# Kernel tuning notes

Hardware: AMD Instinct MI355X
Metric: run time of the kernel (lower is better)

The kernel has to match this reference:

```python
import jax, jax.numpy as jnp
import numpy as np

B = 32768
PASSES = 4

# mask layout: (batch, digit, row, col), values in {0,1}

def _to_lines(m, d):
    """Reorder so the last axis enumerates the 9 cells of a line and axis -2 the 9 lines."""
    if d == 'h':
        return m                      # lines = rows, cells = cols
    if d == 'v':
        return jnp.swapaxes(m, 2, 3)  # lines = cols, cells = rows
    b = m.shape[0]                    # lines = 3x3 boxes
    return m.reshape(b, 9, 3, 3, 3, 3).transpose(0, 1, 2, 4, 3, 5).reshape(b, 9, 9, 9)

_from_lines = _to_lines  # all three reorderings are self-inverse


def filter_line(m, d):
    """SudokuFilterHVBox: remove a solved cell's digit from all other cells in its line."""
    l = _to_lines(m, d)
    cnt = l.sum(axis=1, keepdims=True)                 # candidates per cell
    solved = l * (cnt == 1).astype(l.dtype)            # one-hot solved cells
    other = solved.sum(axis=-1, keepdims=True) - solved  # same digit solved elsewhere in line
    out = l * (other == 0).astype(l.dtype)
    return _from_lines(out, d)


def unique_line(m, d):
    """SudokuUniqueHVBox (hidden single): if a digit fits only one cell in a line, fix it."""
    l = _to_lines(m, d)
    cnt_line = l.sum(axis=-1, keepdims=True)           # per-digit count in the line
    hidden = l * (cnt_line == 1).astype(l.dtype)       # lone placements
    has = hidden.sum(axis=1, keepdims=True) > 0        # cell hosts a hidden single
    out = jnp.where(has, hidden, l)
    return _from_lines(out, d)


def doubles_line(m, d):
    """SudokuDigitsDoubles (naked pair): two identical 2-candidate cells in a line
    eliminate those digits from the rest of the line."""
    l = _to_lines(m, d)                                # (B, d, line, cell)
    cnt = l.sum(axis=1, keepdims=True)
    pm = l * (cnt == 2).astype(l.dtype)                # patterns of 2-candidate cells
    dot = jnp.einsum('bdlc,bdle->blce', pm, pm)        # pattern overlap between cells
    eye = jnp.eye(9, dtype=l.dtype)
    match = (dot == 2).astype(l.dtype) * (1.0 - eye)   # identical pair at another cell
    pairflag = match.sum(-1) > 0                       # (B, line, cell) part of a naked pair
    pair_digit = pm * pairflag[:, None, :, :].astype(l.dtype)
    total_pd = pair_digit.sum(-1, keepdims=True)       # digit belongs to some pair in line
    remove = (total_pd > 0) & (pair_digit == 0)
    out = l * (1.0 - remove.astype(l.dtype))
    return _from_lines(out, d)


def pointing(m, d):
    """SudokuDigitsInOneLineAtBox: if a digit's box candidates lie in one row/col,
    remove that digit from the rest of the row/col outside the box."""
    b = m.shape[0]
    v = m.reshape(b, 9, 3, 3, 3, 3)                    # (B, d, br, ri, bc, ci)
    if d == 'h':
        pres = v.sum(axis=5) > 0                       # (B,d,br,ri,bc) digit in row of box
        nrows = pres.sum(axis=3, keepdims=True)
        point = pres & (nrows == 1)                    # confined to single row within box
        tot = point.sum(axis=4, keepdims=True)         # over bc
        rem = (tot - point) > 0                        # pointing from another box hits us
        out = v * (1.0 - rem[..., None].astype(v.dtype))
    else:
        pres = v.sum(axis=3) > 0                       # (B,d,br,bc,ci) digit in col of box
        ncols = pres.sum(axis=4, keepdims=True)
        point = pres & (ncols == 1)
        tot = point.sum(axis=2, keepdims=True)         # over br
        rem = (tot - point) > 0
        out = v * (1.0 - rem[:, :, :, None, :, :].astype(v.dtype))
    return out.reshape(b, 9, 9, 9)


def _forward_mask(mask):
    for _ in range(PASSES):
        mask = filter_line(mask, 'box')
        mask = pointing(mask, 'h')
        mask = pointing(mask, 'v')
        mask = unique_line(mask, 'h')
        mask = unique_line(mask, 'v')
        mask = unique_line(mask, 'box')
        mask = doubles_line(mask, 'v')   # original code instantiates doubles_h with 'v'
        mask = doubles_line(mask, 'v')
        mask = doubles_line(mask, 'box')
    return mask


def setup_inputs() -> dict:
    key = jax.random.key(0)
    mask = jax.random.randint(key, (B, 9, 9, 9), 0, 2).astype(jnp.float32)
    return {"mask": mask}


def reference(mask):
    out = _forward_mask(mask)
    cnt = out.sum(axis=1)                              # candidates per cell
    solved = jnp.all(cnt == 1, axis=(1, 2))            # (B,) puzzle fully determined
    return (out, solved)
```

## Files before the change

### kernel.cpp

```cpp
#include <hip/hip_runtime.h>
#include <stdint.h>

#define NB 32768
#define NPASS 4
#define FULL27 0x07FFFFFFu
#define NBF (NB * 729)


__device__ __forceinline__ uint32_t colfold(uint32_t w) {
    return (w | (w >> 9) | (w >> 18)) & 0x1FFu;
}
__device__ __forceinline__ uint32_t colmaj2(uint32_t w) {
    return ((w & (w >> 9)) | ((w | (w >> 9)) & (w >> 18))) & 0x1FFu;
}

__global__ __launch_bounds__(256, 1)
void sudoku_kernel(const uint32_t* __restrict__ in, float* __restrict__ out,
                   float* __restrict__ solved) {
    __shared__ uint32_t bpool[1920];
    const int lane = threadIdx.x & 63;
    const int wv   = threadIdx.x >> 6;
    const int trip = lane / 3;
    const int band = lane - trip * 3;
    const int bo1 = band == 2 ? 0 : band + 1;
    const int bo2 = band == 0 ? 2 : band - 1;
    int sl1 = trip * 3 + bo1; if (sl1 > 63) sl1 = 63;
    int sl2 = trip * 3 + bo2; if (sl2 > 63) sl2 = 63;
    const int blockP = blockIdx.x * 84;
    const int pb = blockP + wv * 21;
    const int p = pb + trip;
    const bool valid = (trip < 21) && (p < NB);

    {
        const int base = pb * 729;
        uint32_t* mypool = &bpool[wv * 480];
        #pragma unroll 1
        for (int c = 0; c < 15; ++c) {
            uint32_t v[16];
            #pragma unroll
            for (int j = 0; j < 16; ++j) {
                int gi = base + (c * 16 + j) * 64 + lane;
                if (gi >= NBF) gi = NBF - 1;
                v[j] = in[gi];
            }
            #pragma unroll
            for (int j = 0; j < 16; ++j) {
                unsigned long long m = __ballot(v[j] != 0u);
                if (lane == 0) {
                    int r = c * 16 + j;
                    mypool[2 * r]     = (uint32_t)m;
                    mypool[2 * r + 1] = (uint32_t)(m >> 32);
                }
            }
        }
    }
    __syncthreads();

    uint32_t bd[9];
    {
        const uint32_t* mypool = &bpool[wv * 480];
        const int tx = trip > 20 ? 20 : trip;
        const int bb0 = tx * 729 + band * 27;
        #pragma unroll
        for (int d = 0; d < 9; ++d) {
            int bb = bb0 + d * 81;
            int di = bb >> 5, sh = bb & 31;
            uint64_t both = (uint64_t)mypool[di] | ((uint64_t)mypool[di + 1] << 32);
            bd[d] = (uint32_t)(both >> sh) & FULL27;
        }
    }
    __syncthreads();

    #pragma unroll 1
    for (int pass = 0; pass < NPASS; ++pass) {
        {
            uint32_t on = 0, tw = 0, fo = 0;
            #pragma unroll
            for (int d = 0; d < 9; ++d) {
                uint32_t c = on & bd[d];
                on ^= bd[d]; fo |= tw & c; tw ^= c;
            }
            uint32_t ex1 = on & ~tw & ~fo;
            #pragma unroll
            for (int d = 0; d < 9; ++d) {
                uint32_t s = bd[d] & ex1;
                #pragma unroll
                for (int k = 0; k < 3; ++k) {
                    uint32_t bm = 0x1C0E07u << (3 * k);
                    uint32_t sm = s & bm;
                    uint32_t multi = sm & (sm - 1u);
                    uint32_t keep = (sm == 0u) ? 0xFFFFFFFFu : (~bm | (multi ? 0u : sm));
                    bd[d] &= keep;
                }
            }
        }

        #pragma unroll
        for (int d = 0; d < 9; ++d) {
            uint32_t w = bd[d];
            uint32_t t = (w | (w >> 1) | (w >> 2)) & 0x01249249u;
            uint32_t sum = (t & 0x1FFu) + ((t >> 9) & 0x1FFu) + ((t >> 18) & 0x1FFu);
            uint32_t single = sum & ~(sum >> 1) & 0x49u;
            uint32_t point = t & (single * 0x40201u);
            uint32_t clearm = 0;
            #pragma unroll
            for (int r = 0; r < 3; ++r) {
                uint32_t pr = (point >> (9 * r)) & 0x1FFu;
                uint32_t multi = pr & (pr - 1u);
                uint32_t segkeep = multi ? 0u : pr * 7u;
                uint32_t rc = pr ? ((0x1FFu & ~segkeep) << (9 * r)) : 0u;
                clearm |= rc;
            }
            bd[d] = w & ~clearm;
        }

        {
            uint32_t pnt[9];
            #pragma unroll
            for (int d = 0; d < 9; ++d) {
                uint32_t w = bd[d];
                uint32_t q = colfold(w);
                uint32_t u = (q & 0x49u) + ((q >> 1) & 0x49u) + ((q >> 2) & 0x49u);
                uint32_t single = u & ~(u >> 1) & 0x49u;
                pnt[d] = q & (single * 7u);
            }
            #pragma unroll
            for (int d = 0; d < 9; ++d) {
                uint32_t o = (uint32_t)__shfl((int)pnt[d], sl1, 64) |
                             (uint32_t)__shfl((int)pnt[d], sl2, 64);
                bd[d] &= ~(o * 0x40201u);
            }
        }

        {
            uint32_t hid[9], has = 0;
            #pragma unroll
            for (int d = 0; d < 9; ++d) {
                uint32_t w = bd[d], h = 0;
                #pragma unroll
                for (int r = 0; r < 3; ++r) {
                    uint32_t x = w & (0x1FFu << (9 * r));
                    h |= (x & (x - 1u)) ? 0u : x;
                }
                hid[d] = h; has |= h;
            }
            #pragma unroll
            for (int d = 0; d < 9; ++d) bd[d] = (bd[d] & ~has) | hid[d];
        }

        {
            uint32_t hid[9], has = 0;
            #pragma unroll
            for (int d = 0; d < 9; ++d) {
                uint32_t w = bd[d];
                uint32_t q0 = colfold(w), m0 = colmaj2(w);
                uint32_t ex = q0 | (m0 << 9);
                uint32_t ea = (uint32_t)__shfl((int)ex, sl1, 64);
                uint32_t eb = (uint32_t)__shfl((int)ex, sl2, 64);
                uint32_t qa = ea & 0x1FFu, ma = ea >> 9;
                uint32_t qb = eb & 0x1FFu, mb = eb >> 9;
                uint32_t ge2 = m0 | ma | mb | (q0 & qa) | (q0 & qb) | (qa & qb);
                uint32_t ex1c = (q0 | qa | qb) & ~ge2;
                hid[d] = w & ((ex1c & q0) * 0x40201u);
                has |= hid[d];
            }
            #pragma unroll
            for (int d = 0; d < 9; ++d) bd[d] = (bd[d] & ~has) | hid[d];
        }

        {
            uint32_t hid[9], has = 0;
            #pragma unroll
            for (int d = 0; d < 9; ++d) {
                uint32_t w = bd[d], h = 0;
                #pragma unroll
                for (int k = 0; k < 3; ++k) {
                    uint32_t x = w & (0x1C0E07u << (3 * k));
                    h |= (x & (x - 1u)) ? 0u : x;
                }
                hid[d] = h; has |= h;
            }
            #pragma unroll
            for (int d = 0; d < 9; ++d) bd[d] = (bd[d] & ~has) | hid[d];
        }

        #pragma unroll 1
        for (int rep = 0; rep < 2; ++rep) {
            uint32_t on = 0, tw = 0, fo = 0;
            #pragma unroll
            for (int d = 0; d < 9; ++d) {
                uint32_t c = on & bd[d];
                on ^= bd[d]; fo |= tw & c; tw ^= c;
            }
            uint32_t ex2 = tw & ~on & ~fo;
            uint32_t Q[9], K[9];
            #pragma unroll
            for (int d = 0; d < 9; ++d) { Q[d] = bd[d] & ex2; K[d] = 0u; }
            #pragma unroll
            for (int d1 = 0; d1 < 9; ++d1)
                #pragma unroll
                for (int d2 = d1 + 1; d2 < 9; ++d2) {
                    uint32_t P = Q[d1] & Q[d2];
                    uint32_t f0 = colfold(P), g0 = colmaj2(P);
                    uint32_t ex = f0 | (g0 << 9);
                    uint32_t ea = (uint32_t)__shfl((int)ex, sl1, 64);
                    uint32_t eb = (uint32_t)__shfl((int)ex, sl2, 64);
                    uint32_t fa = ea & 0x1FFu, ga = ea >> 9;
                    uint32_t fb = eb & 0x1FFu, gb = eb >> 9;
                    uint32_t dup = g0 | ga | gb | (f0 & fa) | (f0 & fb) | (fa & fb);
                    uint32_t sK = P & (dup * 0x40201u);
                    K[d1] |= sK; K[d2] |= sK;
                }
            #pragma unroll
            for (int d = 0; d < 9; ++d) {
                uint32_t kc = colfold(K[d]);
                uint32_t cols = kc | (uint32_t)__shfl((int)kc, sl1, 64)
                                   | (uint32_t)__shfl((int)kc, sl2, 64);
                uint32_t em = cols * 0x40201u;
                bd[d] = (bd[d] & ~em) | K[d];
            }
        }

        {
            uint32_t on = 0, tw = 0, fo = 0;
            #pragma unroll
            for (int d = 0; d < 9; ++d) {
                uint32_t c = on & bd[d];
                on ^= bd[d]; fo |= tw & c; tw ^= c;
            }
            uint32_t ex2 = tw & ~on & ~fo;
            uint32_t Q[9], K[9];
            #pragma unroll
            for (int d = 0; d < 9; ++d) { Q[d] = bd[d] & ex2; K[d] = 0u; }
            #pragma unroll
            for (int d1 = 0; d1 < 9; ++d1)
                #pragma unroll
                for (int d2 = d1 + 1; d2 < 9; ++d2) {
                    uint32_t P = Q[d1] & Q[d2];
                    #pragma unroll
                    for (int k = 0; k < 3; ++k) {
                        uint32_t m = P & (0x1C0E07u << (3 * k));
                        uint32_t s = (m & (m - 1u)) ? m : 0u;
                        K[d1] |= s; K[d2] |= s;
                    }
                }
            #pragma unroll
            for (int d = 0; d < 9; ++d)
                #pragma unroll
                for (int k = 0; k < 3; ++k) {
                    uint32_t bm = 0x1C0E07u << (3 * k);
                    uint32_t t = K[d] & bm;
                    uint32_t mask = t ? (~bm | t) : 0xFFFFFFFFu;
                    bd[d] &= mask;
                }
        }
    }

    {
        uint32_t on = 0, tw = 0, fo = 0;
        #pragma unroll
        for (int d = 0; d < 9; ++d) {
            uint32_t c = on & bd[d];
            on ^= bd[d]; fo |= tw & c; tw ^= c;
        }
        uint32_t okb = ((on & ~tw & ~fo) == FULL27) ? 1u : 0u;
        uint32_t all = okb & (uint32_t)__shfl((int)okb, sl1, 64)
                           & (uint32_t)__shfl((int)okb, sl2, 64);
        if (valid && band == 0) solved[p] = all ? 1.0f : 0.0f;
    }

    for (int j = threadIdx.x; j < 1914; j += 256) bpool[j] = 0u;
    __syncthreads();
    if (valid) {
        const int pbit = (wv * 21 + trip) * 729;
        #pragma unroll
        for (int d = 0; d < 9; ++d) {
            int bitbase = pbit + d * 81 + band * 27;
            int di = bitbase >> 5;
            int sh = bitbase & 31;
            uint64_t both = (uint64_t)bd[d] << sh;
            atomicOr(&bpool[di], (uint32_t)both);
            atomicOr(&bpool[di + 1], (uint32_t)(both >> 32));
        }
    }
    __syncthreads();
    {
        int nvb = NB - blockP; if (nvb > 84) nvb = 84;
        const int limit4 = nvb * 729 / 4;
        float4* dst4 = (float4*)(out + (size_t)blockP * 729);
        #pragma unroll 4
        for (int i = 0; i < 60; ++i) {
            int j = i * 256 + (int)threadIdx.x;
            if (j < limit4) {
                uint32_t nib = (bpool[j >> 3] >> ((j & 7) * 4)) & 0xFu;
                dst4[j] = make_float4((float)(nib & 1u), (float)((nib >> 1) & 1u),
                                      (float)((nib >> 2) & 1u), (float)((nib >> 3) & 1u));
            }
        }
    }
}

extern "C" void kernel_launch(void* const* d_in, const int* in_sizes, int n_in,
                              void* d_out, int out_size, void* d_ws, size_t ws_size,
                              hipStream_t stream) {
    const uint32_t* in = (const uint32_t*)d_in[0];
    float* out = (float*)d_out;
    float* solved = out + (size_t)NB * 729;
    sudoku_kernel<<<(NB + 83) / 84, 256, 0, stream>>>(in, out, solved);
}
```

Baseline: 217.0 us.

## Use single-wave blocks with 20 puzzles each instead of 4-wave blocks

Restructures the launch from 256-thread blocks handling 84 puzzles (21 per wave) to 64-thread single-wave blocks handling 20 puzzles each. The load loop is adjusted to cover exactly 20 puzzles' bits (14 chunks plus a 4-row tail), and the output store uses one wave. This raises the block count and lets waves run independently without block-wide syncs across four waves, improving scheduling and latency hiding, at the cost of fewer lanes used per wave (60 of 64 instead of 63).

```diff
diff --git a/kernel.cpp b/kernel.cpp
--- a/kernel.cpp
+++ b/kernel.cpp
@@ -5,6 +5,8 @@
 #define NPASS 4
 #define FULL27 0x07FFFFFFu
 #define NBF (NB * 729)
+#define PPW 20
+#define NBLK ((NB + PPW - 1) / PPW)
 
 
 __device__ __forceinline__ uint32_t colfold(uint32_t w) {
@@ -14,28 +16,25 @@
     return ((w & (w >> 9)) | ((w | (w >> 9)) & (w >> 18))) & 0x1FFu;
 }
 
-__global__ __launch_bounds__(256, 1)
+__global__ __launch_bounds__(64)
 void sudoku_kernel(const uint32_t* __restrict__ in, float* __restrict__ out,
                    float* __restrict__ solved) {
-    __shared__ uint32_t bpool[1920];
-    const int lane = threadIdx.x & 63;
-    const int wv   = threadIdx.x >> 6;
+    __shared__ uint32_t pool[460];
+    const int lane = threadIdx.x;
     const int trip = lane / 3;
     const int band = lane - trip * 3;
     const int bo1 = band == 2 ? 0 : band + 1;
     const int bo2 = band == 0 ? 2 : band - 1;
     int sl1 = trip * 3 + bo1; if (sl1 > 63) sl1 = 63;
     int sl2 = trip * 3 + bo2; if (sl2 > 63) sl2 = 63;
-    const int blockP = blockIdx.x * 84;
-    const int pb = blockP + wv * 21;
-    const int p = pb + trip;
-    const bool valid = (trip < 21) && (p < NB);
+    const int p0 = blockIdx.x * PPW;
+    const int p = p0 + trip;
+    const bool valid = (trip < PPW) && (p < NB);
 
     {
-        const int base = pb * 729;
-        uint32_t* mypool = &bpool[wv * 480];
+        const int base = p0 * 729;
         #pragma unroll 1
-        for (int c = 0; c < 15; ++c) {
+        for (int c = 0; c < 14; ++c) {
             uint32_t v[16];
             #pragma unroll
             for (int j = 0; j < 16; ++j) {
@@ -48,8 +47,26 @@
                 unsigned long long m = __ballot(v[j] != 0u);
                 if (lane == 0) {
                     int r = c * 16 + j;
-                    mypool[2 * r]     = (uint32_t)m;
-                    mypool[2 * r + 1] = (uint32_t)(m >> 32);
+                    pool[2 * r]     = (uint32_t)m;
+                    pool[2 * r + 1] = (uint32_t)(m >> 32);
+                }
+            }
+        }
+        {
+            uint32_t v[4];
+            #pragma unroll
+            for (int j = 0; j < 4; ++j) {
+                int gi = base + (224 + j) * 64 + lane;
+                if (gi >= NBF) gi = NBF - 1;
+                v[j] = in[gi];
+            }
+            #pragma unroll
+            for (int j = 0; j < 4; ++j) {
+                unsigned long long m = __ballot(v[j] != 0u);
+                if (lane == 0) {
+                    int r = 224 + j;
+                    pool[2 * r]     = (uint32_t)m;
+                    pool[2 * r + 1] = (uint32_t)(m >> 32);
                 }
             }
         }
@@ -58,14 +75,13 @@
 
     uint32_t bd[9];
     {
-        const uint32_t* mypool = &bpool[wv * 480];
-        const int tx = trip > 20 ? 20 : trip;
+        const int tx = trip >= PPW ? PPW - 1 : trip;
         const int bb0 = tx * 729 + band * 27;
         #pragma unroll
         for (int d = 0; d < 9; ++d) {
             int bb = bb0 + d * 81;
             int di = bb >> 5, sh = bb & 31;
-            uint64_t both = (uint64_t)mypool[di] | ((uint64_t)mypool[di + 1] << 32);
+            uint64_t both = (uint64_t)pool[di] | ((uint64_t)pool[di + 1] << 32);
             bd[d] = (uint32_t)(both >> sh) & FULL27;
         }
     }
@@ -269,30 +285,30 @@
         if (valid && band == 0) solved[p] = all ? 1.0f : 0.0f;
     }
 
-    for (int j = threadIdx.x; j < 1914; j += 256) bpool[j] = 0u;
+    for (int j = lane; j < 456; j += 64) pool[j] = 0u;
     __syncthreads();
     if (valid) {
-        const int pbit = (wv * 21 + trip) * 729;
+        const int pbit = trip * 729;
         #pragma unroll
         for (int d = 0; d < 9; ++d) {
             int bitbase = pbit + d * 81 + band * 27;
             int di = bitbase >> 5;
             int sh = bitbase & 31;
             uint64_t both = (uint64_t)bd[d] << sh;
-            atomicOr(&bpool[di], (uint32_t)both);
-            atomicOr(&bpool[di + 1], (uint32_t)(both >> 32));
+            atomicOr(&pool[di], (uint32_t)both);
+            atomicOr(&pool[di + 1], (uint32_t)(both >> 32));
         }
     }
     __syncthreads();
     {
-        int nvb = NB - blockP; if (nvb > 84) nvb = 84;
-        const int limit4 = nvb * 729 / 4;
-        float4* dst4 = (float4*)(out + (size_t)blockP * 729);
+        int nv = NB - p0; if (nv > PPW) nv = PPW;
+        const int limit4 = nv * 729 / 4;
+        float4* dst4 = (float4*)(out + (size_t)p0 * 729);
         #pragma unroll 4
-        for (int i = 0; i < 60; ++i) {
-            int j = i * 256 + (int)threadIdx.x;
+        for (int i = 0; i < 57; ++i) {
+            int j = i * 64 + lane;
             if (j < limit4) {
-                uint32_t nib = (bpool[j >> 3] >> ((j & 7) * 4)) & 0xFu;
+                uint32_t nib = (pool[j >> 3] >> ((j & 7) * 4)) & 0xFu;
                 dst4[j] = make_float4((float)(nib & 1u), (float)((nib >> 1) & 1u),
                                       (float)((nib >> 2) & 1u), (float)((nib >> 3) & 1u));
             }
@@ -306,5 +322,5 @@
     const uint32_t* in = (const uint32_t*)d_in[0];
     float* out = (float*)d_out;
     float* solved = out + (size_t)NB * 729;
-    sudoku_kernel<<<(NB + 83) / 84, 256, 0, stream>>>(in, out, solved);
+    sudoku_kernel<<<NBLK, 64, 0, stream>>>(in, out, solved);
 }
```

Result: no change. 216.6 us (median of 2 runs) (-0.2%).
